# Kernel optimization log

Measured on AMD Instinct MI355X. Metric: run time of the kernel, lower is better.

## Reference

```python
import jax, jax.numpy as jnp
import numpy as np
from jax import lax

B, C1, H, W = 512, 64, 15, 15
C = 2 * C1      # fused channels = 128
CR = C // 4     # scAttention reduction = 32
EPS_BN = 1e-5
EPS_COS = 1e-8


def conv2d(x, w, pad, groups=1):
    return lax.conv_general_dilated(x, w, (1, 1), [(pad, pad), (pad, pad)],
                                    feature_group_count=groups,
                                    dimension_numbers=('NCHW', 'OIHW', 'NCHW'))


def batchnorm(x, g, b):
    # training-mode BN: batch statistics over (N, H, W), biased variance
    m = jnp.mean(x, axis=(0, 2, 3), keepdims=True)
    v = jnp.var(x, axis=(0, 2, 3), keepdims=True)
    return (x - m) * lax.rsqrt(v + EPS_BN) * g[None, :, None, None] + b[None, :, None, None]


def setup_inputs() -> dict:
    key = jax.random.key(0)
    ks = jax.random.split(key, 16)
    def n(i, shape, s=0.05):
        return jax.random.normal(ks[i], shape, jnp.float32) * s
    return {
        'x1': jax.random.normal(ks[0], (B, C1, H, W), jnp.float32),
        'x2': jax.random.normal(ks[1], (B, C1, H, W), jnp.float32),
        'lamuda': jnp.asarray(0.5, jnp.float32),
        'bn1_g': jnp.ones((C,), jnp.float32), 'bn1_b': jnp.zeros((C,), jnp.float32),
        'pW1': n(2, (C, C, 1, 1)), 'dW1': n(3, (C, 1, 1, 1)), 'db1': jnp.zeros((C,), jnp.float32),
        'bn2_g': jnp.ones((C,), jnp.float32), 'bn2_b': jnp.zeros((C,), jnp.float32),
        'pW2': n(4, (C, C, 1, 1)), 'dW2': n(5, (C, 1, 3, 3)), 'db2': jnp.zeros((C,), jnp.float32),
        'qkv_W': n(6, (3 * C, C, 1, 1)),
        'bn3_g': jnp.ones((C,), jnp.float32), 'bn3_b': jnp.zeros((C,), jnp.float32),
        'ca_w1': n(7, (CR, C)), 'ca_b1': jnp.zeros((CR,), jnp.float32),
        'ca_w2': n(8, (C, CR)), 'ca_b2': jnp.zeros((C,), jnp.float32),
        'sa_w1': n(9, (CR, C, 7, 7)), 'sa_b1': jnp.zeros((CR,), jnp.float32),
        'sbn1_g': jnp.ones((CR,), jnp.float32), 'sbn1_b': jnp.zeros((CR,), jnp.float32),
        'sa_w2': n(10, (C, CR, 7, 7)), 'sa_b2': jnp.zeros((C,), jnp.float32),
        'sbn2_g': jnp.ones((C,), jnp.float32), 'sbn2_b': jnp.zeros((C,), jnp.float32),
    }


def reference(x1, x2, lamuda, bn1_g, bn1_b, pW1, dW1, db1, bn2_g, bn2_b, pW2, dW2, db2,
              qkv_W, bn3_g, bn3_b, ca_w1, ca_b1, ca_w2, ca_b2,
              sa_w1, sa_b1, sbn1_g, sbn1_b, sa_w2, sa_b2, sbn2_g, sbn2_b):
    x = jnp.concatenate([x1, x2], axis=1)            # (B, C, H, W)
    b, c, h, w = x.shape
    hw = h * w
    cidx = (hw - 1) // 2                             # center pixel index

    # ---- ED_Cos: blended L2-distance + cosine attention vs center spectral vector ----
    q = x.reshape(b, c, hw).transpose(0, 2, 1)       # (B, HW, C)
    cent = q[:, cidx]                                # (B, C)
    e = jnp.sqrt(jnp.sum((q - cent[:, None, :]) ** 2, axis=-1))   # (B, HW)
    sim_e = 1.0 / (1.0 + e)
    qn = jnp.sqrt(jnp.sum(q * q, axis=-1))
    cn = jnp.sqrt(jnp.sum(cent * cent, axis=-1))
    sim_c = jnp.einsum('bc,bpc->bp', cent, q) / (
        jnp.maximum(cn, EPS_COS)[:, None] * jnp.maximum(qn, EPS_COS))
    lmd = jax.nn.sigmoid(lamuda)
    att = lmd * jax.nn.softmax(sim_e, axis=-1) + (1.0 - lmd) * jax.nn.softmax(sim_c, axis=-1)
    # torch .contiguous().view(b,-1,h,w): row-major reinterpret of (B,HW,C) as (B,C,H,W)
    x = (att[:, :, None] * q).reshape(b, c, h, w) + x

    # ---- CSS_Conv 1 (BN -> 1x1 point -> leaky -> 1x1 depthwise -> relu) ----
    y = conv2d(batchnorm(x, bn1_g, bn1_b), pW1, 0)
    y = jnp.where(y >= 0, y, 0.01 * y)               # LeakyReLU(0.01)
    y = conv2d(y, dW1, 0, groups=c) + db1[None, :, None, None]
    x = jax.nn.relu(y)
    # ---- CSS_Conv 2 (BN -> 1x1 point -> leaky -> 3x3 depthwise -> relu) ----
    y = conv2d(batchnorm(x, bn2_g, bn2_b), pW2, 0)
    y = jnp.where(y >= 0, y, 0.01 * y)
    y = conv2d(y, dW2, 1, groups=c) + db2[None, :, None, None]
    x = jax.nn.relu(y)

    # ---- ESSCA.ED: qkv 1x1 conv + L2-distance attention vs center, residual ----
    qkv = conv2d(x, qkv_W, 0).reshape(b, 3 * c, hw).transpose(0, 2, 1)  # (B, HW, 3C)
    qe, ke, ve = jnp.split(qkv, 3, axis=-1)
    cent = qe[:, cidx]
    e = jnp.sqrt(jnp.sum((cent[:, None, :] - ke) ** 2, axis=-1))
    att = jax.nn.softmax(1.0 / (1.0 + e), axis=-1)
    x = (att[:, :, None] * ve).reshape(b, c, h, w) + x

    x = batchnorm(x, bn3_g, bn3_b)

    # ---- scAttention: channel MLP gate then 7x7 spatial gate ----
    xp = x.transpose(0, 2, 3, 1)                     # (B, H, W, C)
    hcatt = jax.nn.relu(xp @ ca_w1.T + ca_b1) @ ca_w2.T + ca_b2
    x = x * jax.nn.sigmoid(hcatt.transpose(0, 3, 1, 2))
    s = jax.nn.relu(batchnorm(conv2d(x, sa_w1, 3) + sa_b1[None, :, None, None], sbn1_g, sbn1_b))
    s = batchnorm(conv2d(s, sa_w2, 3) + sa_b2[None, :, None, None], sbn2_g, sbn2_b)
    return x * jax.nn.sigmoid(s)
```

## Files before the change

### kernel.cpp

```cpp
#include <hip/hip_runtime.h>
#include <hip/hip_bf16.h>
#include <cmath>

#define BB 512
#define CC 128
#define HW 225
#define CIP 136
#define CIPH 40
#define NPMAX 2048
#define NRW 14

typedef __attribute__((ext_vector_type(8))) short short8;
typedef __attribute__((ext_vector_type(4))) float f32x4;
typedef __attribute__((ext_vector_type(4))) unsigned short us4;

union U8 { unsigned short u[8]; short8 v; };

__device__ __forceinline__ unsigned short f2bf(float v) {
  __hip_bfloat16 h = __float2bfloat16(v);
  return *(unsigned short*)&h;
}
__device__ __forceinline__ float bf2f(unsigned short u) {
  __hip_bfloat16 h = *(__hip_bfloat16*)&u;
  return __bfloat162float(h);
}

template<int NT>
__device__ __forceinline__ float br_max(float v, float* red, int t) {
  red[t] = v; __syncthreads();
  for (int st = NT/2; st > 0; st >>= 1) { if (t < st) red[t] = fmaxf(red[t], red[t+st]); __syncthreads(); }
  float r = red[0]; __syncthreads();
  return r;
}
template<int NT>
__device__ __forceinline__ float br_sum(float v, float* red, int t) {
  red[t] = v; __syncthreads();
  for (int st = NT/2; st > 0; st >>= 1) { if (t < st) red[t] += red[t+st]; __syncthreads(); }
  float r = red[0]; __syncthreads();
  return r;
}

__global__ __launch_bounds__(256) void k_bnfin2(const float* __restrict__ ps, const float* __restrict__ pq,
                         int np,
                         const float* __restrict__ g, const float* __restrict__ bt,
                         float* __restrict__ scale, float* __restrict__ shift) {
  int c = blockIdx.x, t = threadIdx.x;
  __shared__ float rs[256], rq[256];
  float s = 0.f, q = 0.f;
  for (int i = t; i < np; i += 256) { s += ps[(size_t)c*NPMAX + i]; q += pq[(size_t)c*NPMAX + i]; }
  rs[t] = s; rq[t] = q; __syncthreads();
  for (int st = 128; st > 0; st >>= 1) { if (t < st) { rs[t]+=rs[t+st]; rq[t]+=rq[t+st]; } __syncthreads(); }
  if (t == 0) {
    const float N = (float)BB*HW;
    float mean = rs[0]/N, var = rq[0]/N - mean*mean;
    float sc = g[c]*rsqrtf(var + 1e-5f);
    scale[c] = sc; shift[c] = bt[c] - mean*sc;
  }
}

__global__ __launch_bounds__(256) void k_at1a(const float* __restrict__ x1, const float* __restrict__ x2,
                       float* __restrict__ part) {
  int b = blockIdx.x, cg = blockIdx.y, t = threadIdx.x;
  __shared__ float cent[32];
  const float* xb1 = x1 + (size_t)b*64*HW;
  const float* xb2 = x2 + (size_t)b*64*HW;
  if (t < 32) { int c = cg*32 + t; cent[t] = (c < 64) ? xb1[c*HW + 112] : xb2[(c-64)*HW + 112]; }
  __syncthreads();
  if (t < HW) {
    float e2 = 0.f, dot = 0.f, qn2 = 0.f;
    for (int k = 0; k < 32; ++k) {
      int c = cg*32 + k;
      float xv = (c < 64) ? xb1[c*HW + t] : xb2[(c-64)*HW + t];
      float ce = cent[k];
      float d = xv - ce;
      e2 += d*d; dot += xv*ce; qn2 += xv*xv;
    }
    size_t base = ((size_t)(b*4 + cg)*3)*256;
    part[base + t] = e2; part[base + 256 + t] = dot; part[base + 512 + t] = qn2;
  }
}

__global__ __launch_bounds__(256) void k_at1b(const float* __restrict__ x1, const float* __restrict__ x2,
                       const float* __restrict__ part, const float* __restrict__ lam,
                       float* __restrict__ am) {
  int b = blockIdx.x, t = threadIdx.x;
  __shared__ float red[256];
  float cv = 0.f;
  if (t < CC) {
    float ce = (t < 64) ? x1[(size_t)b*64*HW + t*HW + 112] : x2[(size_t)b*64*HW + (t-64)*HW + 112];
    cv = ce*ce;
  }
  float cn2 = br_sum<256>(cv, red, t);
  float e2 = 0.f, dot = 0.f, qn2 = 0.f;
  if (t < HW) {
    #pragma unroll
    for (int cg = 0; cg < 4; ++cg) {
      size_t base = ((size_t)(b*4 + cg)*3)*256;
      e2 += part[base + t]; dot += part[base + 256 + t]; qn2 += part[base + 512 + t];
    }
  }
  float sim_e = 0.f, sim_c = 0.f;
  if (t < HW) {
    sim_e = 1.f/(1.f + sqrtf(e2));
    float qn = sqrtf(qn2), cn = sqrtf(cn2);
    sim_c = dot / (fmaxf(cn, 1e-8f) * fmaxf(qn, 1e-8f));
  }
  float m1 = br_max<256>((t<HW)? sim_e : -1e30f, red, t);
  float e1v = (t<HW)? expf(sim_e - m1) : 0.f;
  float s1 = br_sum<256>(e1v, red, t);
  float m2 = br_max<256>((t<HW)? sim_c : -1e30f, red, t);
  float e2v = (t<HW)? expf(sim_c - m2) : 0.f;
  float s2 = br_sum<256>(e2v, red, t);
  float lmd = 1.f/(1.f + expf(-lam[0]));
  if (t < HW) am[(size_t)b*HW + t] = 1.f + lmd*e1v/s1 + (1.f - lmd)*e2v/s2;
}

__global__ __launch_bounds__(256) void k_at1c(const float* __restrict__ x1, const float* __restrict__ x2,
                       const float* __restrict__ am, float* __restrict__ A,
                       float* __restrict__ ps, float* __restrict__ pq) {
  int b = blockIdx.x, cg = blockIdx.y, t = threadIdx.x;
  __shared__ float pS[4][32], pQ[4][32];
  const float* xb1 = x1 + (size_t)b*64*HW;
  const float* xb2 = x2 + (size_t)b*64*HW;
  float* Ab = A + (size_t)b*CC*HW;
  float amv = (t < HW) ? am[(size_t)b*HW + t] : 0.f;
  int w = t >> 6, lane = t & 63;
  for (int k = 0; k < 32; ++k) {
    int c = cg*32 + k;
    float xv = 0.f;
    if (t < HW) xv = (c < 64) ? xb1[c*HW + t] : xb2[(c-64)*HW + t];
    float val = xv*amv;
    if (t < HW) Ab[(size_t)c*HW + t] = val;
    float s = val, q = val*val;
    #pragma unroll
    for (int m = 1; m < 64; m <<= 1) { s += __shfl_xor(s, m); q += __shfl_xor(q, m); }
    if (lane == 0) { pS[w][k] = s; pQ[w][k] = q; }
  }
  __syncthreads();
  if (t < 32) {
    int c = cg*32 + t;
    ps[(size_t)c*NPMAX + b] = pS[0][t]+pS[1][t]+pS[2][t]+pS[3][t];
    pq[(size_t)c*NPMAX + b] = pQ[0][t]+pQ[1][t]+pQ[2][t]+pQ[3][t];
  }
}

__global__ __launch_bounds__(256) void k_prep_all(
    const float* __restrict__ sa_w1, const float* __restrict__ sa_w2,
    const float* __restrict__ pW1, const float* __restrict__ pW2,
    const float* __restrict__ qkvW, const float* __restrict__ ca_w1, const float* __restrict__ ca_w2,
    unsigned short* __restrict__ Wa, unsigned short* __restrict__ Wb,
    unsigned short* __restrict__ W1h, unsigned short* __restrict__ W1l,
    unsigned short* __restrict__ W2h, unsigned short* __restrict__ W2l,
    unsigned short* __restrict__ Wk, unsigned short* __restrict__ Wv,
    unsigned short* __restrict__ Wc1, unsigned short* __restrict__ Wc2) {
  int id = blockIdx.x*256 + threadIdx.x;
  const int NA = 49*4096;
  if (id < NA) {
    int j = id & 7, l = (id >> 3) & 63, ct = (id >> 9) & 1, cs = (id >> 10) & 3, s = id >> 12;
    int co = ct*16 + (l & 15);
    int ci = cs*32 + ((l >> 4) << 3) + j;
    Wa[id] = f2bf(sa_w1[(co*128 + ci)*49 + s]);
    return;
  }
  id -= NA;
  if (id < NA) {
    int j = id & 7, l = (id >> 3) & 63, ct = (id >> 9) & 7, s = id >> 12;
    int co = ct*16 + (l & 15);
    int ci = ((l >> 4) << 3) + j;
    Wb[id] = f2bf(sa_w2[(co*32 + ci)*49 + s]);
    return;
  }
  id -= NA;
  if (id < 16384) {
    int j = id & 7, l = (id >> 3) & 63, ct = (id >> 9) & 7, cs = id >> 12;
    int co = ct*16 + (l & 15);
    int ci = cs*32 + ((l >> 4) << 3) + j;
    float v = pW1[co*128 + ci];
    __hip_bfloat16 h = __float2bfloat16(v);
    W1h[id] = *(unsigned short*)&h;
    W1l[id] = f2bf(v - __bfloat162float(h));
    return;
  }
  id -= 16384;
  if (id < 16384) {
    int j = id & 7, l = (id >> 3) & 63, ct = (id >> 9) & 7, cs = id >> 12;
    int co = ct*16 + (l & 15);
    int ci = cs*32 + ((l >> 4) << 3) + j;
    float v = pW2[co*128 + ci];
    __hip_bfloat16 h = __float2bfloat16(v);
    W2h[id] = *(unsigned short*)&h;
    W2l[id] = f2bf(v - __bfloat162float(h));
    return;
  }
  id -= 16384;
  if (id < 16384) {
    int j = id & 7, l = (id >> 3) & 63, ct = (id >> 9) & 7, cs = id >> 12;
    int co = ct*16 + (l & 15);
    int ci = cs*32 + ((l >> 4) << 3) + j;
    Wk[id] = f2bf(qkvW[(size_t)(128 + co)*128 + ci]);
    Wv[id] = f2bf(qkvW[(size_t)(256 + co)*128 + ci]);
    return;
  }
  id -= 16384;
  if (id < 4096) {
    int j = id & 7, l = (id >> 3) & 63, ct = (id >> 9) & 1, cs = (id >> 10) & 3;
    int co = ct*16 + (l & 15);
    int ci = cs*32 + ((l >> 4) << 3) + j;
    Wc1[id] = f2bf(ca_w1[co*128 + ci]);
    return;
  }
  id -= 4096;
  {
    int j = id & 7, l = (id >> 3) & 63, ct = (id >> 9) & 7;
    int co = ct*16 + (l & 15);
    int ci = ((l >> 4) << 3) + j;
    Wc2[id] = f2bf(ca_w2[co*32 + ci]);
  }
}

template<int MODE>
__global__ __launch_bounds__(256) void k_pw_v3(float* __restrict__ A,
        const unsigned short* __restrict__ Whi, const unsigned short* __restrict__ Wlo,
        const float* __restrict__ scale, const float* __restrict__ shift,
        const float* __restrict__ dw, const float* __restrict__ db,
        float* __restrict__ ps, float* __restrict__ pq) {
  int blk = blockIdx.x;
  int b = blk >> 2, tile = blk & 3, p0 = tile*64;
  int t = threadIdx.x;
  __shared__ __align__(16) unsigned short xh[16*64*8];
  __shared__ __align__(16) unsigned short xl[16*64*8];
  __shared__ float scl[CC], shf[CC], dwl[CC], dbl[CC];
  __shared__ float pS[CC], pQ[CC];
  if (t < CC) {
    scl[t] = scale[t]; shf[t] = shift[t];
    if (MODE == 1) { dwl[t] = dw[t]; dbl[t] = db[t]; }
  }
  __syncthreads();
  float* Ab = A + (size_t)b*CC*HW;
  {
    int px = t & 63, cig = t >> 6;
    int p = p0 + px;
    bool pv = p < HW;
    #pragma unroll
    for (int k0 = 0; k0 < 32; k0 += 8) {
      U8 th, tl;
      #pragma unroll
      for (int j = 0; j < 8; ++j) {
        int ci = cig*32 + k0 + j;
        float v = pv ? Ab[(size_t)ci*HW + p]*scl[ci] + shf[ci] : 0.f;
        __hip_bfloat16 h = __float2bfloat16(v);
        th.u[j] = *(unsigned short*)&h;
        tl.u[j] = f2bf(v - __bfloat162float(h));
      }
      int oo = cig*4 + (k0 >> 3);
      *(short8*)&xh[(oo*64 + px)*8] = th.v;
      *(short8*)&xl[(oo*64 + px)*8] = tl.v;
    }
  }
  __syncthreads();
  int w = t >> 6, l = t & 63, g = l >> 4, n = l & 15;
  const short8* whp = (const short8*)Whi;
  const short8* wlp = (const short8*)Wlo;
  short8 ah[4][2], al[4][2];
  #pragma unroll
  for (int cs = 0; cs < 4; ++cs)
    #pragma unroll
    for (int ctl = 0; ctl < 2; ++ctl) {
      ah[cs][ctl] = whp[(cs*8 + w*2 + ctl)*64 + l];
      al[cs][ctl] = wlp[(cs*8 + w*2 + ctl)*64 + l];
    }
  float ls[2][4] = {}, lq[2][4] = {};
  for (int pt = 0; pt < 4; ++pt) {
    int p = p0 + pt*16 + n;
    bool pv = p < HW;
    short8 bh[4], bl[4];
    #pragma unroll
    for (int cs = 0; cs < 4; ++cs) {
      bh[cs] = *(const short8*)&xh[((cs*4 + g)*64 + pt*16 + n)*8];
      bl[cs] = *(const short8*)&xl[((cs*4 + g)*64 + pt*16 + n)*8];
    }
    f32x4 acc[2] = {};
    #pragma unroll
    for (int cs = 0; cs < 4; ++cs)
      #pragma unroll
      for (int ctl = 0; ctl < 2; ++ctl) {
        acc[ctl] = __builtin_amdgcn_mfma_f32_16x16x32_bf16(ah[cs][ctl], bh[cs], acc[ctl], 0, 0, 0);
        acc[ctl] = __builtin_amdgcn_mfma_f32_16x16x32_bf16(ah[cs][ctl], bl[cs], acc[ctl], 0, 0, 0);
        acc[ctl] = __builtin_amdgcn_mfma_f32_16x16x32_bf16(al[cs][ctl], bh[cs], acc[ctl], 0, 0, 0);
      }
    #pragma unroll
    for (int ctl = 0; ctl < 2; ++ctl)
      #pragma unroll
      for (int r = 0; r < 4; ++r) {
        int co = (w*2 + ctl)*16 + g*4 + r;
        float y = acc[ctl][r];
        y = (y >= 0.f) ? y : 0.01f*y;
        if (MODE == 1) { y = y*dwl[co] + dbl[co]; y = fmaxf(y, 0.f); }
        if (pv) Ab[(size_t)co*HW + p] = y;
        if (MODE == 1) {
          float vs = pv ? y : 0.f;
          ls[ctl][r] += vs; lq[ctl][r] += vs*vs;
        }
      }
  }
  if (MODE == 1) {
    #pragma unroll
    for (int ctl = 0; ctl < 2; ++ctl)
      #pragma unroll
      for (int r = 0; r < 4; ++r) {
        float s = ls[ctl][r], q = lq[ctl][r];
        #pragma unroll
        for (int m = 1; m < 16; m <<= 1) { s += __shfl_xor(s, m); q += __shfl_xor(q, m); }
        if (n == 0) { pS[(w*2 + ctl)*16 + g*4 + r] = s; pQ[(w*2 + ctl)*16 + g*4 + r] = q; }
      }
    __syncthreads();
    if (t < CC) {
      ps[(size_t)t*NPMAX + blk] = pS[t];
      pq[(size_t)t*NPMAX + blk] = pQ[t];
    }
  }
}

__global__ __launch_bounds__(256) void k_dw3(float* __restrict__ A, const float* __restrict__ w,
                      const float* __restrict__ db) {
  int b = blockIdx.x, cg = blockIdx.y, t = threadIdx.x;
  __shared__ float xin[16][HW];
  float* Ab = A + ((size_t)b*CC + cg*16)*HW;
  for (int i = t; i < 16*HW; i += 256) xin[i/HW][i%HW] = Ab[i];
  __syncthreads();
  if (t < HW) {
    int y = t/15, x = t - y*15;
    for (int c = 0; c < 16; ++c) {
      int ch = cg*16 + c;
      float acc = db[ch];
      #pragma unroll
      for (int ky = 0; ky < 3; ++ky) {
        int iy = y + ky - 1;
        if (iy < 0 || iy >= 15) continue;
        #pragma unroll
        for (int kx = 0; kx < 3; ++kx) {
          int ix = x + kx - 1;
          if (ix < 0 || ix >= 15) continue;
          acc += w[ch*9 + ky*3 + kx]*xin[c][iy*15 + ix];
        }
      }
      Ab[c*HW + t] = fmaxf(acc, 0.f);
    }
  }
}

__global__ __launch_bounds__(128) void k_cent(const float* __restrict__ A,
        const float* __restrict__ Wq, float* __restrict__ cent) {
  int b = blockIdx.x, t = threadIdx.x;
  __shared__ float xc[CC];
  const float* Ab = A + (size_t)b*CC*HW;
  xc[t] = bf2f(f2bf(Ab[(size_t)t*HW + 112]));
  __syncthreads();
  const float* wq = Wq + (size_t)t*CC;
  float acc = 0.f;
  for (int ci = 0; ci < CC; ++ci) acc += wq[ci]*xc[ci];
  cent[(size_t)b*CC + t] = acc;
}

__global__ __launch_bounds__(256) void k_attn2a(const float* __restrict__ A,
        const float* __restrict__ cent, const unsigned short* __restrict__ Wk,
        float* __restrict__ sim) {
  int blk = blockIdx.x;
  int b = blk >> 2, tile = blk & 3, p0 = tile*64;
  int t = threadIdx.x;
  __shared__ __align__(16) unsigned short xh[16*64*8];
  __shared__ float cl[CC];
  const float* Ab = A + (size_t)b*CC*HW;
  if (t < CC) cl[t] = cent[(size_t)b*CC + t];
  {
    int px = t & 63, cig = t >> 6;
    int p = p0 + px;
    bool pv = p < HW;
    #pragma unroll
    for (int k0 = 0; k0 < 32; k0 += 8) {
      U8 th;
      #pragma unroll
      for (int j = 0; j < 8; ++j) {
        int ci = cig*32 + k0 + j;
        th.u[j] = pv ? f2bf(Ab[(size_t)ci*HW + p]) : 0;
      }
      *(short8*)&xh[((cig*4 + (k0>>3))*64 + px)*8] = th.v;
    }
  }
  __syncthreads();
  int w = t >> 6, l = t & 63, g = l >> 4, n = l & 15;
  int p = p0 + w*16 + n;
  bool pv = p < HW;
  const short8* wkp = (const short8*)Wk;
  short8 bf[4];
  #pragma unroll
  for (int cs = 0; cs < 4; ++cs)
    bf[cs] = *(const short8*)&xh[((cs*4 + g)*64 + w*16 + n)*8];
  float e2p = 0.f;
  #pragma unroll
  for (int ct = 0; ct < 8; ++ct) {
    f32x4 k = {};
    #pragma unroll
    for (int cs = 0; cs < 4; ++cs)
      k = __builtin_amdgcn_mfma_f32_16x16x32_bf16(wkp[(cs*8 + ct)*64 + l], bf[cs], k, 0, 0, 0);
    #pragma unroll
    for (int r = 0; r < 4; ++r) { float d = cl[ct*16 + g*4 + r] - k[r]; e2p += d*d; }
  }
  e2p += __shfl_xor(e2p, 16);
  e2p += __shfl_xor(e2p, 32);
  if (g == 0 && pv) sim[(size_t)b*HW + p] = 1.f/(1.f + sqrtf(e2p));
}

__global__ __launch_bounds__(256) void k_soft(float* __restrict__ sim) {
  int b = blockIdx.x, t = threadIdx.x;
  __shared__ float red[256];
  float val = (t < HW) ? sim[(size_t)b*HW + t] : -1e30f;
  float m = br_max<256>(val, red, t);
  float e = (t < HW) ? expf(val - m) : 0.f;
  float s = br_sum<256>(e, red, t);
  if (t < HW) sim[(size_t)b*HW + t] = e/s;
}

__global__ __launch_bounds__(256) void k_attn2b(float* __restrict__ A,
        const float* __restrict__ att, const unsigned short* __restrict__ Wv,
        float* __restrict__ ps, float* __restrict__ pq) {
  int blk = blockIdx.x;
  int b = blk >> 2, tile = blk & 3, p0 = tile*64;
  int t = threadIdx.x;
  __shared__ __align__(16) unsigned short xh[16*64*8];
  __shared__ float pS[4][CC], pQ[4][CC];
  float* Ab = A + (size_t)b*CC*HW;
  {
    int px = t & 63, cig = t >> 6;
    int p = p0 + px;
    bool pv = p < HW;
    #pragma unroll
    for (int k0 = 0; k0 < 32; k0 += 8) {
      U8 th;
      #pragma unroll
      for (int j = 0; j < 8; ++j) {
        int ci = cig*32 + k0 + j;
        th.u[j] = pv ? f2bf(Ab[(size_t)ci*HW + p]) : 0;
      }
      *(short8*)&xh[((cig*4 + (k0>>3))*64 + px)*8] = th.v;
    }
  }
  __syncthreads();
  int w = t >> 6, l = t & 63, g = l >> 4, n = l & 15;
  int p = p0 + w*16 + n;
  bool pv = p < HW;
  float ap = pv ? att[(size_t)b*HW + p] : 0.f;
  const short8* wvp = (const short8*)Wv;
  short8 bf[4];
  #pragma unroll
  for (int cs = 0; cs < 4; ++cs)
    bf[cs] = *(const short8*)&xh[((cs*4 + g)*64 + w*16 + n)*8];
  #pragma unroll
  for (int ct = 0; ct < 8; ++ct) {
    f32x4 v = {};
    #pragma unroll
    for (int cs = 0; cs < 4; ++cs)
      v = __builtin_amdgcn_mfma_f32_16x16x32_bf16(wvp[(cs*8 + ct)*64 + l], bf[cs], v, 0, 0, 0);
    #pragma unroll
    for (int r = 0; r < 4; ++r) {
      int co = ct*16 + g*4 + r;
      float val = 0.f;
      if (pv) {
        val = ap*v[r] + Ab[(size_t)co*HW + p];
        Ab[(size_t)co*HW + p] = val;
      }
      float s = val, q = val*val;
      #pragma unroll
      for (int m = 1; m < 16; m <<= 1) { s += __shfl_xor(s, m); q += __shfl_xor(q, m); }
      if (n == 0) { pS[w][co] = s; pQ[w][co] = q; }
    }
  }
  __syncthreads();
  if (t < CC) {
    ps[(size_t)t*NPMAX + blk] = pS[0][t]+pS[1][t]+pS[2][t]+pS[3][t];
    pq[(size_t)t*NPMAX + blk] = pQ[0][t]+pQ[1][t]+pQ[2][t]+pQ[3][t];
  }
}

__global__ __launch_bounds__(256) void k_chatt_v3(const float* __restrict__ A, float* __restrict__ D,
        unsigned short* __restrict__ D2,
        const float* __restrict__ sc, const float* __restrict__ sh,
        const unsigned short* __restrict__ Wc1, const float* __restrict__ b1,
        const unsigned short* __restrict__ Wc2, const float* __restrict__ b2) {
  int blk = blockIdx.x;
  int b = blk >> 2, tile = blk & 3, p0 = tile*64;
  int t = threadIdx.x;
  __shared__ __align__(16) unsigned short xh[16*64*8];
  __shared__ __align__(16) unsigned short hb[64*CIPH];
  __shared__ float scl[CC], shl[CC], b2l[CC], b1l[32];
  const float* Ab = A + (size_t)b*CC*HW;
  float* Db = D + (size_t)b*CC*HW;
  if (t < CC) { scl[t] = sc[t]; shl[t] = sh[t]; b2l[t] = b2[t]; }
  if (t < 32) b1l[t] = b1[t];
  __syncthreads();
  {
    int px = t & 63, cig = t >> 6;
    int p = p0 + px;
    bool pv = p < HW;
    #pragma unroll
    for (int k0 = 0; k0 < 32; k0 += 8) {
      U8 th;
      #pragma unroll
      for (int j = 0; j < 8; ++j) {
        int ci = cig*32 + k0 + j;
        th.u[j] = pv ? f2bf(Ab[(size_t)ci*HW + p]*scl[ci] + shl[ci]) : 0;
      }
      *(short8*)&xh[((cig*4 + (k0>>3))*64 + px)*8] = th.v;
    }
  }
  __syncthreads();
  int w = t >> 6, l = t & 63, g = l >> 4, n = l & 15;
  int p = p0 + w*16 + n;
  bool pv = p < HW;
  const short8* w1p = (const short8*)Wc1;
  const short8* w2p = (const short8*)Wc2;
  short8 bf[4];
  #pragma unroll
  for (int cs = 0; cs < 4; ++cs)
    bf[cs] = *(const short8*)&xh[((cs*4 + g)*64 + w*16 + n)*8];
  #pragma unroll
  for (int ct = 0; ct < 2; ++ct) {
    f32x4 a = {};
    #pragma unroll
    for (int cs = 0; cs < 4; ++cs)
      a = __builtin_amdgcn_mfma_f32_16x16x32_bf16(w1p[(cs*2 + ct)*64 + l], bf[cs], a, 0, 0, 0);
    us4 hv;
    #pragma unroll
    for (int r = 0; r < 4; ++r) hv[r] = f2bf(fmaxf(a[r] + b1l[ct*16 + g*4 + r], 0.f));
    *(us4*)&hb[(w*16+n)*CIPH + ct*16 + g*4] = hv;
  }
  __syncthreads();
  short8 hf = *(const short8*)&hb[(w*16+n)*CIPH + g*8];
  #pragma unroll
  for (int ct = 0; ct < 8; ++ct) {
    f32x4 a = __builtin_amdgcn_mfma_f32_16x16x32_bf16(w2p[ct*64 + l], hf, f32x4{}, 0, 0, 0);
    if (pv) {
      us4 dv;
      #pragma unroll
      for (int r = 0; r < 4; ++r) {
        int co = ct*16 + g*4 + r;
        float s = a[r] + b2l[co];
        float gt = 1.f/(1.f + expf(-s));
        float xin = Ab[(size_t)co*HW + p]*scl[co] + shl[co];
        float o = xin*gt;
        Db[(size_t)co*HW + p] = o;
        dv[r] = f2bf(o);
      }
      if (D2) *(us4*)&D2[((size_t)b*HW + p)*CIP + ct*16 + g*4] = dv;
    }
  }
}

template<int USED2>
__global__ __launch_bounds__(256) void k_conv7a_mfma(const float* __restrict__ D,
        const unsigned short* __restrict__ D2,
        const unsigned short* __restrict__ Wa, float* __restrict__ S,
        float* __restrict__ ps, float* __restrict__ pq) {
  int b = blockIdx.x, half = blockIdx.y, t = threadIdx.x;
  __shared__ __align__(16) unsigned short xb[4*NRW*22*8];
  __shared__ float pS[2][32], pQ[2][32];
  unsigned int* xw = (unsigned int*)xb;
  for (int i = t; i < 4*NRW*22*8/2; i += 256) xw[i] = 0u;
  int w = t >> 6, l = t & 63, g = l >> 4, x = l & 15;
  int ct = w & 1, rh = w >> 1;
  int row0 = half*8;
  f32x4 acc[4] = {};
  const short8* wp = (const short8*)Wa;
  bool prow = false; int rr = 0, xp = 0;
  if (t < HW) {
    int py = t/15, px = t - (t/15)*15;
    int gp = py + 3;
    prow = (gp >= row0) && (gp < row0 + NRW);
    rr = gp - row0; xp = px + 3;
  }
  for (int ck = 0; ck < 4; ++ck) {
    __syncthreads();
    if (prow) {
      if (USED2) {
        const unsigned short* src = &D2[((size_t)b*HW + t)*CIP + ck*32];
        #pragma unroll
        for (int g0 = 0; g0 < 4; ++g0)
          *(short8*)&xb[((g0*NRW + rr)*22 + xp)*8] = *(const short8*)&src[g0*8];
      } else {
        const float* Dbp = D + ((size_t)b*CC + ck*32)*HW;
        #pragma unroll
        for (int g0 = 0; g0 < 4; ++g0) {
          U8 tb;
          #pragma unroll
          for (int k = 0; k < 8; ++k) tb.u[k] = f2bf(Dbp[(g0*8+k)*HW + t]);
          *(short8*)&xb[((g0*NRW + rr)*22 + xp)*8] = tb.v;
        }
      }
    }
    __syncthreads();
    for (int dx = 0; dx < 7; ++dx) {
      short8 aw[7];
      #pragma unroll
      for (int dy = 0; dy < 7; ++dy)
        aw[dy] = wp[(((dy*7 + dx)*4 + ck)*2 + ct)*64 + l];
      #pragma unroll
      for (int rs = 0; rs < 10; ++rs) {
        short8 bf = *(const short8*)&xb[((g*NRW + rh*4 + rs)*22 + x + dx)*8];
        #pragma unroll
        for (int r = 0; r < 4; ++r) {
          int dy = rs - r;
          if (dy >= 0 && dy <= 6)
            acc[r] = __builtin_amdgcn_mfma_f32_16x16x32_bf16(aw[dy], bf, acc[r], 0, 0, 0);
        }
      }
    }
  }
  float ls[4] = {}, lq[4] = {};
  #pragma unroll
  for (int r = 0; r < 4; ++r) {
    int nt = row0 + rh*4 + r;
    bool valid = (x < 15) && (nt < 15);
    if (valid) {
      float* out = S + ((size_t)b*32 + ct*16 + g*4)*HW + nt*15 + x;
      #pragma unroll
      for (int q = 0; q < 4; ++q) out[q*HW] = acc[r][q];
    }
    #pragma unroll
    for (int q = 0; q < 4; ++q) {
      float v = valid ? acc[r][q] : 0.f;
      ls[q] += v; lq[q] += v*v;
    }
  }
  #pragma unroll
  for (int q = 0; q < 4; ++q) {
    float s = ls[q], qq = lq[q];
    #pragma unroll
    for (int m = 1; m < 16; m <<= 1) { s += __shfl_xor(s, m); qq += __shfl_xor(qq, m); }
    if (x == 0) { pS[rh][ct*16 + g*4 + q] = s; pQ[rh][ct*16 + g*4 + q] = qq; }
  }
  __syncthreads();
  if (t < 32) {
    ps[(size_t)t*NPMAX + b*2 + half] = pS[0][t]+pS[1][t];
    pq[(size_t)t*NPMAX + b*2 + half] = pQ[0][t]+pQ[1][t];
  }
}

__global__ __launch_bounds__(256) void k_conv7b_mfma(const float* __restrict__ S,
        const float* __restrict__ sc, const float* __restrict__ sh,
        const unsigned short* __restrict__ Wb, float* __restrict__ O,
        float* __restrict__ ps, float* __restrict__ pq) {
  int b = blockIdx.x, half = blockIdx.y, t = threadIdx.x;
  __shared__ __align__(16) unsigned short xb[4*NRW*22*8];
  __shared__ float scl[32], shl[32];
  __shared__ float pS[CC], pQ[CC];
  unsigned int* xw = (unsigned int*)xb;
  for (int i = t; i < 4*NRW*22*8/2; i += 256) xw[i] = 0u;
  if (t < 32) { scl[t] = sc[t]; shl[t] = sh[t]; }
  __syncthreads();
  int row0 = half*8;
  const float* Sb = S + (size_t)b*32*HW;
  if (t < HW) {
    int py = t/15, px = t - (t/15)*15;
    int gp = py + 3;
    if (gp >= row0 && gp < row0 + NRW) {
      int rr = gp - row0, xp = px + 3;
      #pragma unroll
      for (int g0 = 0; g0 < 4; ++g0) {
        U8 tb;
        #pragma unroll
        for (int k = 0; k < 8; ++k)
          tb.u[k] = f2bf(fmaxf(Sb[(g0*8+k)*HW + t]*scl[g0*8+k] + shl[g0*8+k], 0.f));
        *(short8*)&xb[((g0*NRW + rr)*22 + xp)*8] = tb.v;
      }
    }
  }
  __syncthreads();
  int w = t >> 6, l = t & 63, g = l >> 4, x = l & 15;
  int ct0 = w*2;
  f32x4 acc[2][8] = {};
  const short8* wp = (const short8*)Wb;
  for (int dx = 0; dx < 7; ++dx) {
    short8 a0[7], a1[7];
    #pragma unroll
    for (int dy = 0; dy < 7; ++dy) {
      a0[dy] = wp[((dy*7 + dx)*8 + ct0)*64 + l];
      a1[dy] = wp[((dy*7 + dx)*8 + ct0 + 1)*64 + l];
    }
    #pragma unroll
    for (int rs = 0; rs < 14; ++rs) {
      short8 bf = *(const short8*)&xb[((g*NRW + rs)*22 + x + dx)*8];
      #pragma unroll
      for (int r = 0; r < 8; ++r) {
        int dy = rs - r;
        if (dy >= 0 && dy <= 6) {
          acc[0][r] = __builtin_amdgcn_mfma_f32_16x16x32_bf16(a0[dy], bf, acc[0][r], 0, 0, 0);
          acc[1][r] = __builtin_amdgcn_mfma_f32_16x16x32_bf16(a1[dy], bf, acc[1][r], 0, 0, 0);
        }
      }
    }
  }
  float ls[2][4] = {}, lq[2][4] = {};
  #pragma unroll
  for (int ctl = 0; ctl < 2; ++ctl)
    #pragma unroll
    for (int r = 0; r < 8; ++r) {
      int nt = row0 + r;
      bool valid = (x < 15) && (nt < 15);
      if (valid) {
        float* out = O + ((size_t)b*CC + (ct0+ctl)*16 + g*4)*HW + nt*15 + x;
        #pragma unroll
        for (int q = 0; q < 4; ++q) out[q*HW] = acc[ctl][r][q];
      }
      #pragma unroll
      for (int q = 0; q < 4; ++q) {
        float v = valid ? acc[ctl][r][q] : 0.f;
        ls[ctl][q] += v; lq[ctl][q] += v*v;
      }
    }
  #pragma unroll
  for (int ctl = 0; ctl < 2; ++ctl)
    #pragma unroll
    for (int q = 0; q < 4; ++q) {
      float s = ls[ctl][q], qq = lq[ctl][q];
      #pragma unroll
      for (int m = 1; m < 16; m <<= 1) { s += __shfl_xor(s, m); qq += __shfl_xor(qq, m); }
      if (x == 0) { pS[(ct0+ctl)*16 + g*4 + q] = s; pQ[(ct0+ctl)*16 + g*4 + q] = qq; }
    }
  __syncthreads();
  if (t < CC) {
    ps[(size_t)t*NPMAX + b*2 + half] = pS[t];
    pq[(size_t)t*NPMAX + b*2 + half] = pQ[t];
  }
}

__global__ __launch_bounds__(256) void k_final4(f32x4* __restrict__ D, const f32x4* __restrict__ A,
                        const float* __restrict__ sc, const float* __restrict__ sh) {
  size_t i = (size_t)blockIdx.x*256 + threadIdx.x;
  f32x4 a = A[i], d = D[i];
  size_t e = i*4;
  #pragma unroll
  for (int k = 0; k < 4; ++k) {
    int c = (int)(((e + k) / HW) % CC);
    float s = a[k]*sc[c] + sh[c];
    d[k] *= 1.f/(1.f + expf(-s));
  }
  D[i] = d;
}

extern "C" void kernel_launch(void* const* d_in, const int* in_sizes, int n_in,
                              void* d_out, int out_size, void* d_ws, size_t ws_size,
                              hipStream_t stream) {
  (void)in_sizes; (void)n_in; (void)out_size;
  const float* x1    = (const float*)d_in[0];
  const float* x2    = (const float*)d_in[1];
  const float* lam   = (const float*)d_in[2];
  const float* bn1_g = (const float*)d_in[3];
  const float* bn1_b = (const float*)d_in[4];
  const float* pW1   = (const float*)d_in[5];
  const float* dW1   = (const float*)d_in[6];
  const float* db1   = (const float*)d_in[7];
  const float* bn2_g = (const float*)d_in[8];
  const float* bn2_b = (const float*)d_in[9];
  const float* pW2   = (const float*)d_in[10];
  const float* dW2   = (const float*)d_in[11];
  const float* db2   = (const float*)d_in[12];
  const float* qkvW  = (const float*)d_in[13];
  const float* bn3_g = (const float*)d_in[14];
  const float* bn3_b = (const float*)d_in[15];
  const float* ca_w1 = (const float*)d_in[16];
  const float* ca_b1 = (const float*)d_in[17];
  const float* ca_w2 = (const float*)d_in[18];
  const float* ca_b2 = (const float*)d_in[19];
  const float* sa_w1 = (const float*)d_in[20];
  const float* sbn1_g= (const float*)d_in[22];
  const float* sbn1_b= (const float*)d_in[23];
  const float* sa_w2 = (const float*)d_in[24];
  const float* sbn2_g= (const float*)d_in[26];
  const float* sbn2_b= (const float*)d_in[27];

  float* D = (float*)d_out;
  float* A = (float*)d_ws;
  float* S = A + (size_t)BB*CC*HW;
  float* part = S + (size_t)BB*32*HW;
  float* st = part + (size_t)BB*4*3*256;
  float *sc1 = st,      *sh1 = st+128,  *sc2 = st+256, *sh2 = st+384,
        *sc3 = st+512,  *sh3 = st+640,  *sc4 = st+768, *sh4 = st+800,
        *sc5 = st+832,  *sh5 = st+960;
  float* ps = st + 1280;
  float* pq = ps + (size_t)CC*NPMAX;
  float* cent = pq + (size_t)CC*NPMAX;
  float* sim  = cent + (size_t)BB*CC;
  float* am   = sim + (size_t)BB*HW;
  unsigned short* Wa  = (unsigned short*)(am + (size_t)BB*HW);
  unsigned short* Wb  = Wa + 49*4096;
  unsigned short* W1h = Wb + 49*4096;
  unsigned short* W1l = W1h + 16384;
  unsigned short* W2h = W1l + 16384;
  unsigned short* W2l = W2h + 16384;
  unsigned short* Wk  = W2l + 16384;
  unsigned short* Wv  = Wk  + 16384;
  unsigned short* Wc1 = Wv  + 16384;
  unsigned short* Wc2 = Wc1 + 4096;
  unsigned short* D2  = Wc2 + 4096;
  size_t need = (size_t)((char*)(D2 + (size_t)BB*HW*CIP) - (char*)d_ws);
  bool useD2 = ws_size >= need;

  const int NB4 = BB*4;

  k_prep_all<<<1792, 256, 0, stream>>>(sa_w1, sa_w2, pW1, pW2, qkvW, ca_w1, ca_w2,
                                       Wa, Wb, W1h, W1l, W2h, W2l, Wk, Wv, Wc1, Wc2);

  k_at1a <<<dim3(BB,4), 256, 0, stream>>>(x1, x2, part);
  k_at1b <<<BB, 256, 0, stream>>>(x1, x2, part, lam, am);
  k_at1c <<<dim3(BB,4), 256, 0, stream>>>(x1, x2, am, A, ps, pq);
  k_bnfin2<<<CC, 256, 0, stream>>>(ps, pq, BB, bn1_g, bn1_b, sc1, sh1);
  k_pw_v3<1><<<NB4, 256, 0, stream>>>(A, W1h, W1l, sc1, sh1, dW1, db1, ps, pq);
  k_bnfin2<<<CC, 256, 0, stream>>>(ps, pq, NB4, bn2_g, bn2_b, sc2, sh2);
  k_pw_v3<2><<<NB4, 256, 0, stream>>>(A, W2h, W2l, sc2, sh2, nullptr, nullptr, nullptr, nullptr);
  k_dw3   <<<dim3(BB,8), 256, 0, stream>>>(A, dW2, db2);
  k_cent  <<<BB, 128, 0, stream>>>(A, qkvW, cent);
  k_attn2a<<<NB4, 256, 0, stream>>>(A, cent, Wk, sim);
  k_soft  <<<BB, 256, 0, stream>>>(sim);
  k_attn2b<<<NB4, 256, 0, stream>>>(A, sim, Wv, ps, pq);
  k_bnfin2<<<CC, 256, 0, stream>>>(ps, pq, NB4, bn3_g, bn3_b, sc3, sh3);
  k_chatt_v3<<<NB4, 256, 0, stream>>>(A, D, useD2 ? D2 : nullptr, sc3, sh3, Wc1, ca_b1, Wc2, ca_b2);
  if (useD2) k_conv7a_mfma<1><<<dim3(BB,2), 256, 0, stream>>>(D, D2, Wa, S, ps, pq);
  else       k_conv7a_mfma<0><<<dim3(BB,2), 256, 0, stream>>>(D, nullptr, Wa, S, ps, pq);
  k_bnfin2<<<32, 256, 0, stream>>>(ps, pq, BB*2, sbn1_g, sbn1_b, sc4, sh4);
  k_conv7b_mfma<<<dim3(BB,2), 256, 0, stream>>>(S, sc4, sh4, Wb, A, ps, pq);
  k_bnfin2<<<CC, 256, 0, stream>>>(ps, pq, BB*2, sbn2_g, sbn2_b, sc5, sh5);
  k_final4<<<(BB*CC*HW)/1024, 256, 0, stream>>>((f32x4*)D, (const f32x4*)A, sc5, sh5);
}
```

Before: 548.0 us.

## Process full image per block in 7x7 convs, drop row halves, prefetch chunks

Both 7x7 MFMA conv kernels now handle a whole 15x15 image per block instead of splitting rows across two blocks, which removes the 3-row halo overlap that was loaded and computed twice. conv7a register-prefetches the next input-channel chunk while the current one is computed, and conv7b moves to 512 threads with one channel tile per wave and 15 row accumulators. The aim is fewer redundant MFMAs and less load latency, at the cost of halving the grid to 512 blocks and raising register pressure, which may lower occupancy.

After: 765.5 us. +39.7%, slower.

```diff
diff --git a/kernel.cpp b/kernel.cpp
--- a/kernel.cpp
+++ b/kernel.cpp
@@ -8,7 +8,6 @@
 #define CIP 136
 #define CIPH 40
 #define NPMAX 2048
-#define NRW 14
 
 typedef __attribute__((ext_vector_type(8))) short short8;
 typedef __attribute__((ext_vector_type(4))) float f32x4;
@@ -561,64 +560,84 @@
         const unsigned short* __restrict__ D2,
         const unsigned short* __restrict__ Wa, float* __restrict__ S,
         float* __restrict__ ps, float* __restrict__ pq) {
-  int b = blockIdx.x, half = blockIdx.y, t = threadIdx.x;
-  __shared__ __align__(16) unsigned short xb[4*NRW*22*8];
+  int b = blockIdx.x, t = threadIdx.x;
+  __shared__ __align__(16) unsigned short xb[4*21*22*8];
   __shared__ float pS[2][32], pQ[2][32];
   unsigned int* xw = (unsigned int*)xb;
-  for (int i = t; i < 4*NRW*22*8/2; i += 256) xw[i] = 0u;
+  for (int i = t; i < 4*21*22*8/2; i += 256) xw[i] = 0u;
   int w = t >> 6, l = t & 63, g = l >> 4, x = l & 15;
   int ct = w & 1, rh = w >> 1;
-  int row0 = half*8;
-  f32x4 acc[4] = {};
+  int base = rh*8;
+  f32x4 acc[8] = {};
   const short8* wp = (const short8*)Wa;
-  bool prow = false; int rr = 0, xp = 0;
+  int pr = 0;
+  if (t < HW) { int py = t/15, px = t - (t/15)*15; pr = (py+3)*22 + (px+3); }
+  short8 stg[4];
   if (t < HW) {
-    int py = t/15, px = t - (t/15)*15;
-    int gp = py + 3;
-    prow = (gp >= row0) && (gp < row0 + NRW);
-    rr = gp - row0; xp = px + 3;
+    if (USED2) {
+      const unsigned short* src = &D2[((size_t)b*HW + t)*CIP];
+      #pragma unroll
+      for (int g0 = 0; g0 < 4; ++g0) stg[g0] = *(const short8*)&src[g0*8];
+    } else {
+      const float* Dbp = D + (size_t)b*CC*HW;
+      #pragma unroll
+      for (int g0 = 0; g0 < 4; ++g0) {
+        U8 tb;
+        #pragma unroll
+        for (int k = 0; k < 8; ++k) tb.u[k] = f2bf(Dbp[(g0*8+k)*HW + t]);
+        stg[g0] = tb.v;
+      }
+    }
   }
   for (int ck = 0; ck < 4; ++ck) {
     __syncthreads();
-    if (prow) {
-      if (USED2) {
-        const unsigned short* src = &D2[((size_t)b*HW + t)*CIP + ck*32];
-        #pragma unroll
-        for (int g0 = 0; g0 < 4; ++g0)
-          *(short8*)&xb[((g0*NRW + rr)*22 + xp)*8] = *(const short8*)&src[g0*8];
-      } else {
-        const float* Dbp = D + ((size_t)b*CC + ck*32)*HW;
-        #pragma unroll
-        for (int g0 = 0; g0 < 4; ++g0) {
-          U8 tb;
+    if (t < HW) {
+      #pragma unroll
+      for (int g0 = 0; g0 < 4; ++g0)
+        *(short8*)&xb[(g0*21*22 + pr)*8] = stg[g0];
+    }
+    __syncthreads();
+    if (ck < 3) {
+      if (t < HW) {
+        if (USED2) {
+          const unsigned short* src = &D2[((size_t)b*HW + t)*CIP + (ck+1)*32];
           #pragma unroll
-          for (int k = 0; k < 8; ++k) tb.u[k] = f2bf(Dbp[(g0*8+k)*HW + t]);
-          *(short8*)&xb[((g0*NRW + rr)*22 + xp)*8] = tb.v;
+          for (int g0 = 0; g0 < 4; ++g0) stg[g0] = *(const short8*)&src[g0*8];
+        } else {
+          const float* Dbp = D + ((size_t)b*CC + (ck+1)*32)*HW;
+          #pragma unroll
+          for (int g0 = 0; g0 < 4; ++g0) {
+            U8 tb;
+            #pragma unroll
+            for (int k = 0; k < 8; ++k) tb.u[k] = f2bf(Dbp[(g0*8+k)*HW + t]);
+            stg[g0] = tb.v;
+          }
         }
       }
     }
-    __syncthreads();
     for (int dx = 0; dx < 7; ++dx) {
       short8 aw[7];
       #pragma unroll
       for (int dy = 0; dy < 7; ++dy)
         aw[dy] = wp[(((dy*7 + dx)*4 + ck)*2 + ct)*64 + l];
       #pragma unroll
-      for (int rs = 0; rs < 10; ++rs) {
-        short8 bf = *(const short8*)&xb[((g*NRW + rh*4 + rs)*22 + x + dx)*8];
-        #pragma unroll
-        for (int r = 0; r < 4; ++r) {
-          int dy = rs - r;
-          if (dy >= 0 && dy <= 6)
-            acc[r] = __builtin_amdgcn_mfma_f32_16x16x32_bf16(aw[dy], bf, acc[r], 0, 0, 0);
+      for (int rs = 0; rs < 14; ++rs) {
+        if (base + rs < 21) {
+          short8 bf = *(const short8*)&xb[((g*21 + base + rs)*22 + x + dx)*8];
+          #pragma unroll
+          for (int r = 0; r < 8; ++r) {
+            int dy = rs - r;
+            if (dy >= 0 && dy <= 6)
+              acc[r] = __builtin_amdgcn_mfma_f32_16x16x32_bf16(aw[dy], bf, acc[r], 0, 0, 0);
+          }
         }
       }
     }
   }
   float ls[4] = {}, lq[4] = {};
   #pragma unroll
-  for (int r = 0; r < 4; ++r) {
-    int nt = row0 + rh*4 + r;
+  for (int r = 0; r < 8; ++r) {
+    int nt = base + r;
     bool valid = (x < 15) && (nt < 15);
     if (valid) {
       float* out = S + ((size_t)b*32 + ct*16 + g*4)*HW + nt*15 + x;
@@ -640,96 +659,83 @@
   }
   __syncthreads();
   if (t < 32) {
-    ps[(size_t)t*NPMAX + b*2 + half] = pS[0][t]+pS[1][t];
-    pq[(size_t)t*NPMAX + b*2 + half] = pQ[0][t]+pQ[1][t];
-  }
-}
-
-__global__ __launch_bounds__(256) void k_conv7b_mfma(const float* __restrict__ S,
+    ps[(size_t)t*NPMAX + b] = pS[0][t]+pS[1][t];
+    pq[(size_t)t*NPMAX + b] = pQ[0][t]+pQ[1][t];
+  }
+}
+
+__global__ __launch_bounds__(512) void k_conv7b_mfma(const float* __restrict__ S,
         const float* __restrict__ sc, const float* __restrict__ sh,
         const unsigned short* __restrict__ Wb, float* __restrict__ O,
         float* __restrict__ ps, float* __restrict__ pq) {
-  int b = blockIdx.x, half = blockIdx.y, t = threadIdx.x;
-  __shared__ __align__(16) unsigned short xb[4*NRW*22*8];
+  int b = blockIdx.x, t = threadIdx.x;
+  __shared__ __align__(16) unsigned short xb[4*21*22*8];
   __shared__ float scl[32], shl[32];
   __shared__ float pS[CC], pQ[CC];
   unsigned int* xw = (unsigned int*)xb;
-  for (int i = t; i < 4*NRW*22*8/2; i += 256) xw[i] = 0u;
+  for (int i = t; i < 4*21*22*8/2; i += 512) xw[i] = 0u;
   if (t < 32) { scl[t] = sc[t]; shl[t] = sh[t]; }
   __syncthreads();
-  int row0 = half*8;
   const float* Sb = S + (size_t)b*32*HW;
   if (t < HW) {
     int py = t/15, px = t - (t/15)*15;
-    int gp = py + 3;
-    if (gp >= row0 && gp < row0 + NRW) {
-      int rr = gp - row0, xp = px + 3;
-      #pragma unroll
-      for (int g0 = 0; g0 < 4; ++g0) {
-        U8 tb;
-        #pragma unroll
-        for (int k = 0; k < 8; ++k)
-          tb.u[k] = f2bf(fmaxf(Sb[(g0*8+k)*HW + t]*scl[g0*8+k] + shl[g0*8+k], 0.f));
-        *(short8*)&xb[((g0*NRW + rr)*22 + xp)*8] = tb.v;
-      }
+    int pr = (py+3)*22 + (px+3);
+    #pragma unroll
+    for (int g0 = 0; g0 < 4; ++g0) {
+      U8 tb;
+      #pragma unroll
+      for (int k = 0; k < 8; ++k)
+        tb.u[k] = f2bf(fmaxf(Sb[(g0*8+k)*HW + t]*scl[g0*8+k] + shl[g0*8+k], 0.f));
+      *(short8*)&xb[(g0*21*22 + pr)*8] = tb.v;
     }
   }
   __syncthreads();
   int w = t >> 6, l = t & 63, g = l >> 4, x = l & 15;
-  int ct0 = w*2;
-  f32x4 acc[2][8] = {};
+  int ct = w;
+  f32x4 acc[15] = {};
   const short8* wp = (const short8*)Wb;
   for (int dx = 0; dx < 7; ++dx) {
-    short8 a0[7], a1[7];
-    #pragma unroll
-    for (int dy = 0; dy < 7; ++dy) {
-      a0[dy] = wp[((dy*7 + dx)*8 + ct0)*64 + l];
-      a1[dy] = wp[((dy*7 + dx)*8 + ct0 + 1)*64 + l];
-    }
-    #pragma unroll
-    for (int rs = 0; rs < 14; ++rs) {
-      short8 bf = *(const short8*)&xb[((g*NRW + rs)*22 + x + dx)*8];
-      #pragma unroll
-      for (int r = 0; r < 8; ++r) {
+    short8 aw[7];
+    #pragma unroll
+    for (int dy = 0; dy < 7; ++dy)
+      aw[dy] = wp[((dy*7 + dx)*8 + ct)*64 + l];
+    #pragma unroll
+    for (int rs = 0; rs < 21; ++rs) {
+      short8 bf = *(const short8*)&xb[((g*21 + rs)*22 + x + dx)*8];
+      #pragma unroll
+      for (int r = 0; r < 15; ++r) {
         int dy = rs - r;
-        if (dy >= 0 && dy <= 6) {
-          acc[0][r] = __builtin_amdgcn_mfma_f32_16x16x32_bf16(a0[dy], bf, acc[0][r], 0, 0, 0);
-          acc[1][r] = __builtin_amdgcn_mfma_f32_16x16x32_bf16(a1[dy], bf, acc[1][r], 0, 0, 0);
-        }
-      }
-    }
-  }
-  float ls[2][4] = {}, lq[2][4] = {};
-  #pragma unroll
-  for (int ctl = 0; ctl < 2; ++ctl)
-    #pragma unroll
-    for (int r = 0; r < 8; ++r) {
-      int nt = row0 + r;
-      bool valid = (x < 15) && (nt < 15);
-      if (valid) {
-        float* out = O + ((size_t)b*CC + (ct0+ctl)*16 + g*4)*HW + nt*15 + x;
-        #pragma unroll
-        for (int q = 0; q < 4; ++q) out[q*HW] = acc[ctl][r][q];
-      }
-      #pragma unroll
-      for (int q = 0; q < 4; ++q) {
-        float v = valid ? acc[ctl][r][q] : 0.f;
-        ls[ctl][q] += v; lq[ctl][q] += v*v;
-      }
-    }
-  #pragma unroll
-  for (int ctl = 0; ctl < 2; ++ctl)
+        if (dy >= 0 && dy <= 6)
+          acc[r] = __builtin_amdgcn_mfma_f32_16x16x32_bf16(aw[dy], bf, acc[r], 0, 0, 0);
+      }
+    }
+  }
+  float ls[4] = {}, lq[4] = {};
+  #pragma unroll
+  for (int r = 0; r < 15; ++r) {
+    bool valid = (x < 15);
+    if (valid) {
+      float* out = O + ((size_t)b*CC + ct*16 + g*4)*HW + r*15 + x;
+      #pragma unroll
+      for (int q = 0; q < 4; ++q) out[q*HW] = acc[r][q];
+    }
     #pragma unroll
     for (int q = 0; q < 4; ++q) {
-      float s = ls[ctl][q], qq = lq[ctl][q];
-      #pragma unroll
-      for (int m = 1; m < 16; m <<= 1) { s += __shfl_xor(s, m); qq += __shfl_xor(qq, m); }
-      if (x == 0) { pS[(ct0+ctl)*16 + g*4 + q] = s; pQ[(ct0+ctl)*16 + g*4 + q] = qq; }
-    }
+      float v = valid ? acc[r][q] : 0.f;
+      ls[q] += v; lq[q] += v*v;
+    }
+  }
+  #pragma unroll
+  for (int q = 0; q < 4; ++q) {
+    float s = ls[q], qq = lq[q];
+    #pragma unroll
+    for (int m = 1; m < 16; m <<= 1) { s += __shfl_xor(s, m); qq += __shfl_xor(qq, m); }
+    if (x == 0) { pS[ct*16 + g*4 + q] = s; pQ[ct*16 + g*4 + q] = qq; }
+  }
   __syncthreads();
   if (t < CC) {
-    ps[(size_t)t*NPMAX + b*2 + half] = pS[t];
-    pq[(size_t)t*NPMAX + b*2 + half] = pQ[t];
+    ps[(size_t)t*NPMAX + b] = pS[t];
+    pq[(size_t)t*NPMAX + b] = pQ[t];
   }
 }
 
@@ -824,10 +830,10 @@
   k_attn2b<<<NB4, 256, 0, stream>>>(A, sim, Wv, ps, pq);
   k_bnfin2<<<CC, 256, 0, stream>>>(ps, pq, NB4, bn3_g, bn3_b, sc3, sh3);
   k_chatt_v3<<<NB4, 256, 0, stream>>>(A, D, useD2 ? D2 : nullptr, sc3, sh3, Wc1, ca_b1, Wc2, ca_b2);
-  if (useD2) k_conv7a_mfma<1><<<dim3(BB,2), 256, 0, stream>>>(D, D2, Wa, S, ps, pq);
-  else       k_conv7a_mfma<0><<<dim3(BB,2), 256, 0, stream>>>(D, nullptr, Wa, S, ps, pq);
-  k_bnfin2<<<32, 256, 0, stream>>>(ps, pq, BB*2, sbn1_g, sbn1_b, sc4, sh4);
-  k_conv7b_mfma<<<dim3(BB,2), 256, 0, stream>>>(S, sc4, sh4, Wb, A, ps, pq);
-  k_bnfin2<<<CC, 256, 0, stream>>>(ps, pq, BB*2, sbn2_g, sbn2_b, sc5, sh5);
+  if (useD2) k_conv7a_mfma<1><<<BB, 256, 0, stream>>>(D, D2, Wa, S, ps, pq);
+  else       k_conv7a_mfma<0><<<BB, 256, 0, stream>>>(D, nullptr, Wa, S, ps, pq);
+  k_bnfin2<<<32, 256, 0, stream>>>(ps, pq, BB, sbn1_g, sbn1_b, sc4, sh4);
+  k_conv7b_mfma<<<BB, 512, 0, stream>>>(S, sc4, sh4, Wb, A, ps, pq);
+  k_bnfin2<<<CC, 256, 0, stream>>>(ps, pq, BB, sbn2_g, sbn2_b, sc5, sh5);
   k_final4<<<(BB*CC*HW)/1024, 256, 0, stream>>>((f32x4*)D, (const f32x4*)A, sc5, sh5);
 }
```
